# Performance work log

Measured on AMD Instinct MI355X. Metric: run time of the kernel, lower is better.

The kernel has to match this reference:

```python
import jax, jax.numpy as jnp
import numpy as np

N_NODES = 100000
N_EDGES = 1200000
N_HOP = 3
DIM = 64
EPS = 1e-5


def _bn(x):
    # BatchNorm1d over nodes, train-mode stats, gamma=1, beta=0
    m = x.mean(axis=0)
    v = x.var(axis=0)
    return (x - m) / jnp.sqrt(v + EPS)


def _gcn_conv(x, W, b, src, dst, n):
    # PyG GCNConv: add self-loops, symmetric deg^-1/2 (A+I) deg^-1/2, then bias
    xw = x @ W                                            # [N, D]
    deg = jax.ops.segment_sum(jnp.ones_like(src, dtype=xw.dtype), dst,
                              num_segments=n) + 1.0       # self-loop adds 1
    dinv = jax.lax.rsqrt(deg)                             # deg >= 1
    coef = dinv[src] * dinv[dst]                          # [E]
    agg = jax.ops.segment_sum(xw[src] * coef[:, None], dst, num_segments=n)
    agg = agg + (dinv * dinv)[:, None] * xw               # self-loop message
    return agg + b


def setup_inputs() -> dict:
    key = jax.random.key(0)
    ks = jax.random.split(key, 8)
    backbone_outputs = jax.random.normal(ks[0], (4, N_NODES, DIM), dtype=jnp.float32)
    khop_edge_index = jax.random.randint(ks[1], (N_HOP, 2, N_EDGES), 0, N_NODES)
    comb_w = jax.random.normal(ks[2], (N_HOP + 1, 3), dtype=jnp.float32)
    ego_W = jax.random.normal(ks[3], (DIM, DIM), dtype=jnp.float32) / np.sqrt(DIM)
    ego_b = jnp.zeros((DIM,), dtype=jnp.float32)
    conv_W = jax.random.normal(ks[4], (N_HOP, DIM, DIM), dtype=jnp.float32) / np.sqrt(DIM)
    conv_b = jnp.zeros((N_HOP, DIM), dtype=jnp.float32)
    return {"backbone_outputs": backbone_outputs, "comb_w": comb_w,
            "ego_W": ego_W, "ego_b": ego_b, "conv_W": conv_W, "conv_b": conv_b,
            "khop_edge_index": khop_edge_index}


def reference(backbone_outputs, comb_w, ego_W, ego_b, conv_W, conv_b, khop_edge_index):
    n = backbone_outputs.shape[1]
    # SimpleCombine: softmax-weighted mixes of backbone layer outputs (skip input)
    w = jax.nn.softmax(comb_w, axis=1)                    # [n_hop+1, 3]
    multi = jnp.einsum('ji,ind->jnd', w, backbone_outputs[1:])  # [n_hop+1, N, D]
    # ego path: linear -> BN (dropout=0)
    hidden = _bn(multi[0] @ ego_W + ego_b)
    for k in range(N_HOP):
        src = khop_edge_index[k, 0]
        dst = khop_edge_index[k, 1]
        prop = _gcn_conv(multi[k + 1], conv_W[k], conv_b[k], src, dst, n)
        hidden = hidden + jax.nn.relu(_bn(prop))
    return jax.nn.log_softmax(hidden, axis=1)
```

## Files before the change

kernel.cpp:

```cpp
#include <hip/hip_runtime.h>
#include <hip/hip_bf16.h>

#define NND 100000
#define NED 1200000
#define NHOP 3
#define DM 64
#define EPSV 1e-5f
#define NB1 391

typedef long long i64;

__device__ __forceinline__ float rlf(float v, int k) {
    return __builtin_bit_cast(float, __builtin_amdgcn_readlane(__builtin_bit_cast(int, v), k));
}

__global__ void k_weights(const float* __restrict__ comb_w, float* __restrict__ wsoft) {
    int j = threadIdx.x;
    if (j < NHOP + 1) {
        float a0 = comb_w[j * 3 + 0], a1 = comb_w[j * 3 + 1], a2 = comb_w[j * 3 + 2];
        float mx = fmaxf(a0, fmaxf(a1, a2));
        float e0 = expf(a0 - mx), e1 = expf(a1 - mx), e2 = expf(a2 - mx);
        float s = 1.0f / (e0 + e1 + e2);
        wsoft[j * 3 + 0] = e0 * s; wsoft[j * 3 + 1] = e1 * s; wsoft[j * 3 + 2] = e2 * s;
    }
}

__global__ __launch_bounds__(256) void k_gemm(const float* __restrict__ bb,
                                              const float* __restrict__ wsoft, int j,
                                              const float* __restrict__ W,
                                              const float* __restrict__ dinv, int scale,
                                              float* __restrict__ stats, int dostats,
                                              float* __restrict__ xw) {
    const int lane = threadIdx.x & 63;
    float Wcol[DM];
#pragma unroll
    for (int k = 0; k < DM; k++) Wcol[k] = W[k * DM + lane];
    const float w0 = wsoft[j * 3 + 0], w1 = wsoft[j * 3 + 1], w2 = wsoft[j * 3 + 2];
    const float* b1 = bb + (i64)1 * NND * DM;
    const float* b2 = bb + (i64)2 * NND * DM;
    const float* b3 = bb + (i64)3 * NND * DM;
    int wave = (int)((blockIdx.x * blockDim.x + threadIdx.x) >> 6);
    int nw = (int)((gridDim.x * blockDim.x) >> 6);
    float s = 0.f, sq = 0.f;
    for (int n = wave; n < NND; n += nw) {
        i64 base = (i64)n * DM + lane;
        float m = w0 * b1[base] + w1 * b2[base] + w2 * b3[base];
        float a0 = 0.f, a1 = 0.f, a2 = 0.f, a3 = 0.f;
#pragma unroll
        for (int k = 0; k < DM; k += 4) {
            a0 = fmaf(rlf(m, k + 0), Wcol[k + 0], a0);
            a1 = fmaf(rlf(m, k + 1), Wcol[k + 1], a1);
            a2 = fmaf(rlf(m, k + 2), Wcol[k + 2], a2);
            a3 = fmaf(rlf(m, k + 3), Wcol[k + 3], a3);
        }
        float r = (a0 + a1) + (a2 + a3);
        if (scale) r *= dinv[n];
        xw[base] = r;
        s += r; sq += r * r;
    }
    if (dostats) {
        __shared__ float ls[4][DM], lq[4][DM];
        int row = threadIdx.x >> 6;
        ls[row][lane] = s; lq[row][lane] = sq;
        __syncthreads();
        if (row == 0) {
            s  = ls[0][lane] + ls[1][lane] + ls[2][lane] + ls[3][lane];
            sq = lq[0][lane] + lq[1][lane] + lq[2][lane] + lq[3][lane];
            unsafeAtomicAdd(&stats[lane], s);
            unsafeAtomicAdd(&stats[DM + lane], sq);
        }
    }
}

__global__ __launch_bounds__(256) void k_deg(const int* __restrict__ dst, int* __restrict__ deg) {
    int i = blockIdx.x * blockDim.x + threadIdx.x;
    int stride = gridDim.x * blockDim.x;
    for (int e = i; e < NED; e += stride) atomicAdd(&deg[dst[e]], 1);
}

__global__ __launch_bounds__(256) void k_scan1(const int* __restrict__ deg,
                                               int* __restrict__ off,
                                               int* __restrict__ partials,
                                               float* __restrict__ dinv) {
    int t = threadIdx.x;
    int n = blockIdx.x * 256 + t;
    int d = (n < NND) ? deg[n] : 0;
    if (n < NND) dinv[n] = rsqrtf((float)d + 1.0f);
    __shared__ int sh[256];
    sh[t] = d;
    __syncthreads();
    for (int o = 1; o < 256; o <<= 1) {
        int v = (t >= o) ? sh[t - o] : 0;
        __syncthreads();
        sh[t] += v;
        __syncthreads();
    }
    if (n < NND) off[n] = sh[t] - d;
    if (t == 255) partials[blockIdx.x] = sh[255];
}

__global__ __launch_bounds__(512) void k_scan2(int* __restrict__ partials) {
    int t = threadIdx.x;
    int d = (t < NB1) ? partials[t] : 0;
    __shared__ int sh[512];
    sh[t] = d;
    __syncthreads();
    for (int o = 1; o < 512; o <<= 1) {
        int v = (t >= o) ? sh[t - o] : 0;
        __syncthreads();
        sh[t] += v;
        __syncthreads();
    }
    if (t < NB1) partials[t] = sh[t] - d;
}

__global__ __launch_bounds__(256) void k_scan3(int* __restrict__ off,
                                               const int* __restrict__ partials) {
    int n = blockIdx.x * 256 + threadIdx.x;
    if (n < NND) off[n] += partials[blockIdx.x];
}

__global__ __launch_bounds__(256) void k_bucket(const int* __restrict__ src,
                                                const int* __restrict__ dst,
                                                const int* __restrict__ off,
                                                int* __restrict__ cursor,
                                                int* __restrict__ sortedsrc) {
    int i = blockIdx.x * blockDim.x + threadIdx.x;
    int stride = gridDim.x * blockDim.x;
    for (int e = i; e < NED; e += stride) {
        int d = dst[e];
        int pos = off[d] + atomicAdd(&cursor[d], 1);
        sortedsrc[pos] = src[e];
    }
}

__global__ __launch_bounds__(256) void k_gather(const float* __restrict__ xws,
                                                const int* __restrict__ sortedsrc,
                                                const int* __restrict__ off,
                                                const int* __restrict__ deg,
                                                const float* __restrict__ dinv,
                                                float* __restrict__ xbuf,
                                                float* __restrict__ stats) {
    const int lane = threadIdx.x & 63;
    int wave = (int)((blockIdx.x * blockDim.x + threadIdx.x) >> 6);
    int nw = (int)((gridDim.x * blockDim.x) >> 6);
    float s = 0.f, sq = 0.f;
    for (int n = wave; n < NND; n += nw) {
        float acc = xws[(i64)n * DM + lane];
        int start = off[n];
        int cnt = deg[n];
        int i = 0;
        while (i < cnt) {
            int m = cnt - i; if (m > 64) m = 64;
            int sl = (lane < m) ? sortedsrc[start + i + lane] : 0;
            for (int t = 0; t < m; t++) {
                int ss = __builtin_amdgcn_readlane(sl, t);
                acc += xws[(i64)ss * DM + lane];
            }
            i += m;
        }
        float x = acc * dinv[n];
        xbuf[(i64)n * DM + lane] = x;
        s += x; sq += x * x;
    }
    __shared__ float ls[4][DM], lq[4][DM];
    int row = threadIdx.x >> 6;
    ls[row][lane] = s; lq[row][lane] = sq;
    __syncthreads();
    if (row == 0) {
        s  = ls[0][lane] + ls[1][lane] + ls[2][lane] + ls[3][lane];
        sq = lq[0][lane] + lq[1][lane] + lq[2][lane] + lq[3][lane];
        unsafeAtomicAdd(&stats[lane], s);
        unsafeAtomicAdd(&stats[DM + lane], sq);
    }
}

__global__ __launch_bounds__(256) void k_apply(const float* __restrict__ xbuf, int mode,
                                               const float* __restrict__ stats,
                                               float* __restrict__ hidden,
                                               float* __restrict__ out) {
    const int lane = threadIdx.x & 63;
    float mean = stats[lane] * (1.0f / NND);
    float var = stats[DM + lane] * (1.0f / NND) - mean * mean;
    float inv = rsqrtf(var + EPSV);
    int wave = (int)((blockIdx.x * blockDim.x + threadIdx.x) >> 6);
    int nw = (int)((gridDim.x * blockDim.x) >> 6);
    for (int n = wave; n < NND; n += nw) {
        i64 i = (i64)n * DM + lane;
        float bn = (xbuf[i] - mean) * inv;
        if (mode == 0) {
            hidden[i] = bn;
        } else if (mode == 1) {
            hidden[i] += fmaxf(bn, 0.0f);
        } else {
            float h = hidden[i] + fmaxf(bn, 0.0f);
            float mx = h;
#pragma unroll
            for (int off = 32; off >= 1; off >>= 1) mx = fmaxf(mx, __shfl_xor(mx, off));
            float e = expf(h - mx);
            float ssum = e;
#pragma unroll
            for (int off = 32; off >= 1; off >>= 1) ssum += __shfl_xor(ssum, off);
            out[i] = h - mx - logf(ssum);
        }
    }
}

extern "C" void kernel_launch(void* const* d_in, const int* in_sizes, int n_in,
                              void* d_out, int out_size, void* d_ws, size_t ws_size,
                              hipStream_t stream) {
    const float* bb     = (const float*)d_in[0];
    const float* comb_w = (const float*)d_in[1];
    const float* ego_W  = (const float*)d_in[2];
    const float* conv_W = (const float*)d_in[4];
    const int*   edges  = (const int*)d_in[6];
    float* out = (float*)d_out;

    const i64 NF = (i64)NND * DM;
    char* ws = (char*)d_ws;
    float* wsoft     = (float*)ws;
    float* stats     = wsoft + 64;
    float* xws       = stats + 128;
    float* xbuf      = xws + NF;
    float* dinv      = xbuf + NF;
    int*   deg       = (int*)(dinv + NND);
    int*   off       = deg + NND;
    int*   cursor    = off + NND;
    int*   partials  = cursor + NND;
    int*   sortedsrc = partials + 512;
    float* hidden = out;

    k_weights<<<1, 64, 0, stream>>>(comb_w, wsoft);

    hipMemsetAsync(stats, 0, 2 * DM * sizeof(float), stream);
    k_gemm<<<1024, 256, 0, stream>>>(bb, wsoft, 0, ego_W, dinv, 0, stats, 1, xws);
    k_apply<<<512, 256, 0, stream>>>(xws, 0, stats, hidden, out);

    for (int k = 0; k < NHOP; k++) {
        const int* src = edges + (i64)k * 2 * NED;
        const int* dst = src + NED;
        hipMemsetAsync(deg, 0, NND * sizeof(int), stream);
        hipMemsetAsync(cursor, 0, NND * sizeof(int), stream);
        hipMemsetAsync(stats, 0, 2 * DM * sizeof(float), stream);
        k_deg<<<1024, 256, 0, stream>>>(dst, deg);
        k_scan1<<<NB1, 256, 0, stream>>>(deg, off, partials, dinv);
        k_scan2<<<1, 512, 0, stream>>>(partials);
        k_scan3<<<NB1, 256, 0, stream>>>(off, partials);
        k_bucket<<<1024, 256, 0, stream>>>(src, dst, off, cursor, sortedsrc);
        k_gemm<<<1024, 256, 0, stream>>>(bb, wsoft, k + 1, conv_W + (i64)k * DM * DM,
                                         dinv, 1, stats, 0, xws);
        k_gather<<<2048, 256, 0, stream>>>(xws, sortedsrc, off, deg, dinv, xbuf, stats);
        int mode = (k == NHOP - 1) ? 2 : 1;
        k_apply<<<512, 256, 0, stream>>>(xbuf, mode, stats, hidden, out);
    }
}
```

Baseline: 1.016 ms.

## Store projected features in bf16, fuse ego BN into first apply, drop scan3/cursor

```diff
diff --git a/kernel.cpp b/kernel.cpp
--- a/kernel.cpp
+++ b/kernel.cpp
@@ -9,9 +9,18 @@
 #define NB1 391
 
 typedef long long i64;
+typedef unsigned short u16;
+typedef unsigned int u32;
 
 __device__ __forceinline__ float rlf(float v, int k) {
     return __builtin_bit_cast(float, __builtin_amdgcn_readlane(__builtin_bit_cast(int, v), k));
+}
+__device__ __forceinline__ float bf2f(u16 b) {
+    return __builtin_bit_cast(float, (u32)b << 16);
+}
+__device__ __forceinline__ u16 f2bf(float f) {
+    u32 u = __builtin_bit_cast(u32, f);
+    return (u16)((u + 0x7FFFu + ((u >> 16) & 1u)) >> 16);
 }
 
 __global__ void k_weights(const float* __restrict__ comb_w, float* __restrict__ wsoft) {
@@ -30,7 +39,7 @@
                                               const float* __restrict__ W,
                                               const float* __restrict__ dinv, int scale,
                                               float* __restrict__ stats, int dostats,
-                                              float* __restrict__ xw) {
+                                              u16* __restrict__ xw) {
     const int lane = threadIdx.x & 63;
     float Wcol[DM];
 #pragma unroll
@@ -55,7 +64,7 @@
         }
         float r = (a0 + a1) + (a2 + a3);
         if (scale) r *= dinv[n];
-        xw[base] = r;
+        xw[base] = f2bf(r);
         s += r; sq += r * r;
     }
     if (dostats) {
@@ -114,29 +123,24 @@
     if (t < NB1) partials[t] = sh[t] - d;
 }
 
-__global__ __launch_bounds__(256) void k_scan3(int* __restrict__ off,
-                                               const int* __restrict__ partials) {
-    int n = blockIdx.x * 256 + threadIdx.x;
-    if (n < NND) off[n] += partials[blockIdx.x];
-}
-
 __global__ __launch_bounds__(256) void k_bucket(const int* __restrict__ src,
                                                 const int* __restrict__ dst,
-                                                const int* __restrict__ off,
-                                                int* __restrict__ cursor,
+                                                int* __restrict__ off,
+                                                const int* __restrict__ partials,
                                                 int* __restrict__ sortedsrc) {
     int i = blockIdx.x * blockDim.x + threadIdx.x;
     int stride = gridDim.x * blockDim.x;
     for (int e = i; e < NED; e += stride) {
         int d = dst[e];
-        int pos = off[d] + atomicAdd(&cursor[d], 1);
+        int pos = partials[d >> 8] + atomicAdd(&off[d], 1);
         sortedsrc[pos] = src[e];
     }
 }
 
-__global__ __launch_bounds__(256) void k_gather(const float* __restrict__ xws,
+__global__ __launch_bounds__(256) void k_gather(const u16* __restrict__ xws,
                                                 const int* __restrict__ sortedsrc,
                                                 const int* __restrict__ off,
+                                                const int* __restrict__ partials,
                                                 const int* __restrict__ deg,
                                                 const float* __restrict__ dinv,
                                                 float* __restrict__ xbuf,
@@ -146,16 +150,28 @@
     int nw = (int)((gridDim.x * blockDim.x) >> 6);
     float s = 0.f, sq = 0.f;
     for (int n = wave; n < NND; n += nw) {
-        float acc = xws[(i64)n * DM + lane];
-        int start = off[n];
         int cnt = deg[n];
+        int start = partials[n >> 8] + off[n] - cnt;
+        float acc = bf2f(xws[(i64)n * DM + lane]);
         int i = 0;
         while (i < cnt) {
             int m = cnt - i; if (m > 64) m = 64;
             int sl = (lane < m) ? sortedsrc[start + i + lane] : 0;
-            for (int t = 0; t < m; t++) {
+            int t = 0;
+            for (; t + 4 <= m; t += 4) {
+                int s0 = __builtin_amdgcn_readlane(sl, t + 0);
+                int s1 = __builtin_amdgcn_readlane(sl, t + 1);
+                int s2 = __builtin_amdgcn_readlane(sl, t + 2);
+                int s3 = __builtin_amdgcn_readlane(sl, t + 3);
+                float v0 = bf2f(xws[(i64)s0 * DM + lane]);
+                float v1 = bf2f(xws[(i64)s1 * DM + lane]);
+                float v2 = bf2f(xws[(i64)s2 * DM + lane]);
+                float v3 = bf2f(xws[(i64)s3 * DM + lane]);
+                acc += ((v0 + v1) + (v2 + v3));
+            }
+            for (; t < m; t++) {
                 int ss = __builtin_amdgcn_readlane(sl, t);
-                acc += xws[(i64)ss * DM + lane];
+                acc += bf2f(xws[(i64)ss * DM + lane]);
             }
             i += m;
         }
@@ -175,32 +191,41 @@
     }
 }
 
-__global__ __launch_bounds__(256) void k_apply(const float* __restrict__ xbuf, int mode,
-                                               const float* __restrict__ stats,
+__global__ __launch_bounds__(256) void k_apply(const float* __restrict__ xbuf,
+                                               const u16* __restrict__ xwsA, int mode,
+                                               const float* __restrict__ statsA,
+                                               const float* __restrict__ statsB,
                                                float* __restrict__ hidden,
                                                float* __restrict__ out) {
     const int lane = threadIdx.x & 63;
-    float mean = stats[lane] * (1.0f / NND);
-    float var = stats[DM + lane] * (1.0f / NND) - mean * mean;
-    float inv = rsqrtf(var + EPSV);
+    float meanB = statsB[lane] * (1.0f / NND);
+    float varB = statsB[DM + lane] * (1.0f / NND) - meanB * meanB;
+    float invB = rsqrtf(varB + EPSV);
+    float meanA = 0.f, invA = 0.f;
+    if (mode == 0) {
+        meanA = statsA[lane] * (1.0f / NND);
+        float varA = statsA[DM + lane] * (1.0f / NND) - meanA * meanA;
+        invA = rsqrtf(varA + EPSV);
+    }
     int wave = (int)((blockIdx.x * blockDim.x + threadIdx.x) >> 6);
     int nw = (int)((gridDim.x * blockDim.x) >> 6);
     for (int n = wave; n < NND; n += nw) {
         i64 i = (i64)n * DM + lane;
-        float bn = (xbuf[i] - mean) * inv;
+        float bn = (xbuf[i] - meanB) * invB;
+        float r = fmaxf(bn, 0.0f);
         if (mode == 0) {
-            hidden[i] = bn;
+            hidden[i] = (bf2f(xwsA[i]) - meanA) * invA + r;
         } else if (mode == 1) {
-            hidden[i] += fmaxf(bn, 0.0f);
+            hidden[i] += r;
         } else {
-            float h = hidden[i] + fmaxf(bn, 0.0f);
+            float h = hidden[i] + r;
             float mx = h;
 #pragma unroll
-            for (int off = 32; off >= 1; off >>= 1) mx = fmaxf(mx, __shfl_xor(mx, off));
+            for (int o = 32; o >= 1; o >>= 1) mx = fmaxf(mx, __shfl_xor(mx, o));
             float e = expf(h - mx);
             float ssum = e;
 #pragma unroll
-            for (int off = 32; off >= 1; off >>= 1) ssum += __shfl_xor(ssum, off);
+            for (int o = 32; o >= 1; o >>= 1) ssum += __shfl_xor(ssum, o);
             out[i] = h - mx - logf(ssum);
         }
     }
@@ -220,37 +245,34 @@
     char* ws = (char*)d_ws;
     float* wsoft     = (float*)ws;
     float* stats     = wsoft + 64;
-    float* xws       = stats + 128;
-    float* xbuf      = xws + NF;
+    u16*   xwsA      = (u16*)(stats + 512);
+    u16*   xwsB      = xwsA + NF;
+    float* xbuf      = (float*)(xwsB + NF);
     float* dinv      = xbuf + NF;
     int*   deg       = (int*)(dinv + NND);
     int*   off       = deg + NND;
-    int*   cursor    = off + NND;
-    int*   partials  = cursor + NND;
+    int*   partials  = off + NND;
     int*   sortedsrc = partials + 512;
     float* hidden = out;
 
     k_weights<<<1, 64, 0, stream>>>(comb_w, wsoft);
-
-    hipMemsetAsync(stats, 0, 2 * DM * sizeof(float), stream);
-    k_gemm<<<1024, 256, 0, stream>>>(bb, wsoft, 0, ego_W, dinv, 0, stats, 1, xws);
-    k_apply<<<512, 256, 0, stream>>>(xws, 0, stats, hidden, out);
+    hipMemsetAsync(stats, 0, 4 * 128 * sizeof(float), stream);
+
+    k_gemm<<<1024, 256, 0, stream>>>(bb, wsoft, 0, ego_W, dinv, 0, stats, 1, xwsA);
 
     for (int k = 0; k < NHOP; k++) {
         const int* src = edges + (i64)k * 2 * NED;
         const int* dst = src + NED;
+        float* statsB = stats + (k + 1) * 128;
         hipMemsetAsync(deg, 0, NND * sizeof(int), stream);
-        hipMemsetAsync(cursor, 0, NND * sizeof(int), stream);
-        hipMemsetAsync(stats, 0, 2 * DM * sizeof(float), stream);
         k_deg<<<1024, 256, 0, stream>>>(dst, deg);
         k_scan1<<<NB1, 256, 0, stream>>>(deg, off, partials, dinv);
         k_scan2<<<1, 512, 0, stream>>>(partials);
-        k_scan3<<<NB1, 256, 0, stream>>>(off, partials);
-        k_bucket<<<1024, 256, 0, stream>>>(src, dst, off, cursor, sortedsrc);
         k_gemm<<<1024, 256, 0, stream>>>(bb, wsoft, k + 1, conv_W + (i64)k * DM * DM,
-                                         dinv, 1, stats, 0, xws);
-        k_gather<<<2048, 256, 0, stream>>>(xws, sortedsrc, off, deg, dinv, xbuf, stats);
-        int mode = (k == NHOP - 1) ? 2 : 1;
-        k_apply<<<512, 256, 0, stream>>>(xbuf, mode, stats, hidden, out);
-    }
-}
+                                         dinv, 1, statsB, 0, xwsB);
+        k_bucket<<<1024, 256, 0, stream>>>(src, dst, off, partials, sortedsrc);
+        k_gather<<<4096, 256, 0, stream>>>(xwsB, sortedsrc, off, partials, deg, dinv,
+                                           xbuf, statsB);
+        k_apply<<<512, 256, 0, stream>>>(xbuf, xwsA, k, stats, statsB, hidden, out);
+    }
+}
```

Measured after the change: 1.087 ms. 1.07x slower.
